# Performance work log

Hardware: AMD Instinct MI355X
Metric: run time of the kernel (lower is better)

The kernel has to match this reference:

```python
import jax, jax.numpy as jnp
import numpy as np

RADIUS = 0.3
NEIGHBOR_LIMIT = 32
LN_EPS = 1e-5


def setup_inputs() -> dict:
    key = jax.random.key(0)
    k0, k1, k2 = jax.random.split(key, 3)
    N, C = 16384, 256
    pts = jax.random.normal(k0, (N, 3), jnp.float32)
    masks = jnp.ones((N,), dtype=bool)  # all queries active (fixed shape for jit)
    feats = jax.random.normal(k1, (N, C), jnp.float32)
    W = jax.random.normal(k2, (C, C), jnp.float32) * (1.0 / np.sqrt(C))
    b = jnp.zeros((C,), jnp.float32)
    gamma = jnp.ones((C,), jnp.float32)
    beta = jnp.zeros((C,), jnp.float32)
    return {
        "shifted_src_points_c": pts,
        "src_masks": masks,
        "src_feats_c": feats,
        "W": W,
        "b": b,
        "gamma": gamma,
        "beta": beta,
    }


def _ball_query(q, s, radius, k):
    # squared pairwise distances via the ||q||^2 + ||s||^2 - 2 q.s^T identity
    # (avoids the [N, N, 3] broadcast intermediate)
    q2 = jnp.sum(q * q, axis=-1, keepdims=True)        # [Q, 1]
    s2 = jnp.sum(s * s, axis=-1)                        # [N]
    d2 = q2 + s2[None, :] - 2.0 * (q @ s.T)             # [Q, N]
    neg_d2, idx = jax.lax.top_k(-d2, k)                 # k nearest neighbors
    # out-of-radius slots get index 0, matching the original
    # `neighbor_indices[neighbor_indices == N] = 0` padding replacement
    idx = jnp.where(-neg_d2 > radius * radius, 0, idx)
    return idx                                          # [Q, k] int32


def reference(shifted_src_points_c, src_masks, src_feats_c, W, b, gamma, beta):
    # src_masks is all-True by construction -> queries == all points
    q_nodes = shifted_src_points_c
    idx = _ball_query(q_nodes, shifted_src_points_c, RADIUS, NEIGHBOR_LIMIT)
    group = src_feats_c[idx]                            # [Q, K, C] irregular gather
    pooled = jnp.max(group, axis=1)                     # max over neighbors -> [Q, C]
    h = pooled @ W.T + b                                # nn.Linear(256, 256)
    mu = jnp.mean(h, axis=-1, keepdims=True)
    var = jnp.var(h, axis=-1, keepdims=True)
    h = (h - mu) * jax.lax.rsqrt(var + LN_EPS) * gamma + beta  # LayerNorm
    return jax.nn.relu(h)
```

## Files before the change

kernel.cpp:

```cpp
#include <hip/hip_runtime.h>
#include <stdint.h>

#define NPTS 16384
#define CFEAT 256
#define KNN 32
#define RR_HI 0.0900101f
#define NC 21
#define NCELLS (NC * NC * NC)
#define NPAD 9264
#define INVW 3.3332222f
#define NBUCK 128

typedef __attribute__((ext_vector_type(8))) short short8;
typedef __attribute__((ext_vector_type(4))) float floatx4;

__device__ __forceinline__ uint32_t f2bf(uint32_t u) {
  return (u + 0x7fffu + ((u >> 16) & 1u)) >> 16;
}
__device__ __forceinline__ int cell1d(float x) {
  int c = (int)floorf((x + 3.15f) * INVW);
  return min(max(c, 0), NC - 1);
}

__global__ __launch_bounds__(256) void k_prep(const float* __restrict__ feats,
                                              uint16_t* __restrict__ featsb,
                                              const float* __restrict__ Wm,
                                              uint16_t* __restrict__ Wb,
                                              const float* __restrict__ pts,
                                              uint32_t* __restrict__ cellcnt) {
  const int b = blockIdx.x, t = threadIdx.x;
  if (b < 4096) {
    const int i = b * 256 + t;
    const uint4 u = ((const uint4*)feats)[i];
    const uint32_t lo = f2bf(u.x) | (f2bf(u.y) << 16);
    const uint32_t hi = f2bf(u.z) | (f2bf(u.w) << 16);
    ((uint2*)featsb)[i] = make_uint2(lo, hi);
  } else {
    const int i = (b - 4096) * 256 + t;
    const uint4 u = ((const uint4*)Wm)[i];
    const uint32_t lo = f2bf(u.x) | (f2bf(u.y) << 16);
    const uint32_t hi = f2bf(u.z) | (f2bf(u.w) << 16);
    ((uint2*)Wb)[i] = make_uint2(lo, hi);
    const int cx = cell1d(pts[3 * i]), cy = cell1d(pts[3 * i + 1]), cz = cell1d(pts[3 * i + 2]);
    atomicAdd(&cellcnt[(cz * NC + cy) * NC + cx], 1u);
  }
}

__global__ __launch_bounds__(1024) void k_scan(const uint32_t* __restrict__ hist,
                                               uint32_t* __restrict__ start, int n) {
  __shared__ uint32_t wsum[16];
  __shared__ uint32_t carry;
  const int t = threadIdx.x, wv = t >> 6, ln = t & 63;
  if (t == 0) carry = 0;
  __syncthreads();
  const int nq = n >> 2;
  for (int qb = 0; qb < nq; qb += 4096) {
    uint4 v[4];
    uint32_t psum[4];
    uint32_t tot = 0;
    #pragma unroll
    for (int k = 0; k < 4; ++k) {
      const int i4 = qb + t * 4 + k;
      v[k] = (i4 < nq) ? ((const uint4*)hist)[i4] : make_uint4(0, 0, 0, 0);
      psum[k] = tot;
      tot += v[k].x + v[k].y + v[k].z + v[k].w;
    }
    uint32_t s = tot;
    #pragma unroll
    for (int off = 1; off < 64; off <<= 1) {
      uint32_t o = __shfl_up(s, off, 64);
      if (ln >= off) s += o;
    }
    if (ln == 63) wsum[wv] = s;
    const uint32_t cbase = carry;
    __syncthreads();
    uint32_t woff = 0;
    for (int w = 0; w < wv; ++w) woff += wsum[w];
    const uint32_t base = cbase + woff + s - tot;
    #pragma unroll
    for (int k = 0; k < 4; ++k) {
      const int i4 = qb + t * 4 + k;
      if (i4 < nq) {
        const uint32_t e = base + psum[k];
        ((uint4*)start)[i4] =
            make_uint4(e, e + v[k].x, e + v[k].x + v[k].y, e + v[k].x + v[k].y + v[k].z);
      }
    }
    __syncthreads();
    if (t == 1023) carry = base + tot;
    __syncthreads();
  }
  if (t == 0) start[n] = carry;
}

__global__ __launch_bounds__(256) void k_scatter(const float* __restrict__ pts,
                                                 const uint32_t* __restrict__ cellstart,
                                                 uint32_t* __restrict__ cellptr,
                                                 uint32_t* __restrict__ sortedq,
                                                 float4* __restrict__ sortedpts) {
  const int i = blockIdx.x * 256 + threadIdx.x;
  const float x = pts[3 * i], y = pts[3 * i + 1], z = pts[3 * i + 2];
  const int c = (cell1d(z) * NC + cell1d(y)) * NC + cell1d(x);
  const uint32_t pos = cellstart[c] + atomicAdd(&cellptr[c], 1u);
  sortedq[pos] = (uint32_t)i;
  sortedpts[pos] = make_float4(x, y, z, __uint_as_float((uint32_t)i));
}

__global__ __launch_bounds__(256) void k_fsp(const uint32_t* __restrict__ sortedq,
                                             const uint32_t* __restrict__ cellstart,
                                             const float4* __restrict__ sortedpts,
                                             const uint16_t* __restrict__ featsb,
                                             uint16_t* __restrict__ pooledb) {
  __shared__ uint64_t keys[4][256];
  __shared__ uint32_t hist[4][NBUCK];
  __shared__ uint32_t sids[4][KNN];
  const int t = threadIdx.x;
  const int w = t >> 6;
  const int lane = t & 63;
  const uint64_t ltmask = (1ull << lane) - 1ull;
  const int q = (int)sortedq[blockIdx.x * 4 + w];
  const float4 qp = sortedpts[blockIdx.x * 4 + w];
  const float qx = qp.x, qy = qp.y, qz = qp.z;
  const int icx = cell1d(qx), icy = cell1d(qy), icz = cell1d(qz);
  const int x0 = max(icx - 1, 0), x1 = min(icx + 1, NC - 1);
  int S[9], E[9];
  #pragma unroll
  for (int r = 0; r < 9; ++r) {
    const int cz = icz + (r / 3) - 1;
    const int cy = icy + (r % 3) - 1;
    const bool ok = (cz >= 0) && (cz < NC) && (cy >= 0) && (cy < NC);
    const int rb = ((ok ? cz : 0) * NC + (ok ? cy : 0)) * NC;
    const int s = (int)cellstart[rb + x0];
    const int e = (int)cellstart[rb + x1 + 1];
    S[r] = ok ? s : 0;
    E[r] = ok ? e : 0;
  }
  int PRE[10], OFF[9];
  PRE[0] = 0;
  #pragma unroll
  for (int r = 0; r < 9; ++r) {
    PRE[r + 1] = PRE[r] + (E[r] - S[r]);
    OFF[r] = S[r] - PRE[r];
  }
  const int total = PRE[9];
  uint32_t c_run = 0;
  for (int v0 = 0; v0 < total; v0 += 64) {
    const int v = v0 + lane;
    int addr = v + OFF[0];
    #pragma unroll
    for (int r = 1; r < 9; ++r) addr = (v >= PRE[r]) ? (v + OFF[r]) : addr;
    const int ia = min(addr, NPTS - 1);
    const float4 p = sortedpts[ia];
    const float dxf = qx - p.x, dyf = qy - p.y, dzf = qz - p.z;
    const float d2 = __fmaf_rn(dxf, dxf, __fmaf_rn(dyf, dyf, __fmul_rn(dzf, dzf)));
    bool pass = (v < total) && (d2 <= RR_HI);
    uint64_t key = 0;
    if (pass) {
      const double ddx = (double)qx - (double)p.x;
      const double ddy = (double)qy - (double)p.y;
      const double ddz = (double)qz - (double)p.z;
      const double dd2 = fma(ddx, ddx, fma(ddy, ddy, ddz * ddz));
      pass = (dd2 <= 0.3 * 0.3);
      key = ((uint64_t)__double_as_longlong(dd2) & ~0x3FFFull) |
            (uint64_t)__float_as_uint(p.w);
    }
    const uint64_t mask = __ballot(pass);
    if (pass) {
      const uint32_t pos = c_run + (uint32_t)__popcll(mask & ltmask);
      if (pos < 256u) keys[w][pos] = key;
    }
    c_run += (uint32_t)__popcll(mask);
  }
  const int c = (int)min(c_run, 256u);
  if (c <= KNN) {
    if (lane < KNN) sids[w][lane] = (lane < c) ? (uint32_t)(keys[w][lane] & 0x3FFFull) : 0u;
  } else {
    const uint64_t INVALID = ~0ull;
    uint64_t k0 = (lane < c) ? keys[w][lane] : INVALID;
    uint64_t k1 = (lane + 64 < c) ? keys[w][lane + 64] : INVALID;
    uint64_t k2 = (lane + 128 < c) ? keys[w][lane + 128] : INVALID;
    uint64_t k3 = (lane + 192 < c) ? keys[w][lane + 192] : INVALID;
    hist[w][lane] = 0;
    hist[w][lane + 64] = 0;
    int b0 = 999, b1 = 999, b2 = 999, b3 = 999;
    const float bs = 128.0f / 0.09f;
    if (k0 != INVALID) { b0 = min(NBUCK - 1, (int)((float)__longlong_as_double((long long)(k0 & ~0x3FFFull)) * bs)); atomicAdd(&hist[w][b0], 1u); }
    if (k1 != INVALID) { b1 = min(NBUCK - 1, (int)((float)__longlong_as_double((long long)(k1 & ~0x3FFFull)) * bs)); atomicAdd(&hist[w][b1], 1u); }
    if (k2 != INVALID) { b2 = min(NBUCK - 1, (int)((float)__longlong_as_double((long long)(k2 & ~0x3FFFull)) * bs)); atomicAdd(&hist[w][b2], 1u); }
    if (k3 != INVALID) { b3 = min(NBUCK - 1, (int)((float)__longlong_as_double((long long)(k3 & ~0x3FFFull)) * bs)); atomicAdd(&hist[w][b3], 1u); }
    const uint32_t h0 = hist[w][2 * lane], h1 = hist[w][2 * lane + 1];
    const uint32_t tot = h0 + h1;
    uint32_t s = tot;
    #pragma unroll
    for (int off = 1; off < 64; off <<= 1) {
      uint32_t o = __shfl_up(s, off, 64);
      if (lane >= off) s += o;
    }
    const uint32_t C0 = s - tot + h0;
    const uint32_t C1 = s - tot + h0 + h1;
    const uint64_t me = __ballot(C0 >= KNN);
    const uint64_t mo = __ballot(C1 >= KNN);
    const int be = me ? 2 * (__ffsll((unsigned long long)me) - 1) : (1 << 30);
    const int bo = mo ? 2 * (__ffsll((unsigned long long)mo) - 1) + 1 : (1 << 30);
    const int bstar = min(be, bo);
    const uint32_t mval_mine = (bstar & 1) ? (C1 - h1) : (C0 - h0);
    const uint32_t m = (uint32_t)__shfl((int)mval_mine, bstar >> 1, 64);
    uint32_t wpos = 0;
    {
      bool win = (b0 < bstar);
      uint64_t bm = __ballot(win);
      if (win) sids[w][wpos + (uint32_t)__popcll(bm & ltmask)] = (uint32_t)(k0 & 0x3FFFull);
      wpos += (uint32_t)__popcll(bm);
      win = (b1 < bstar); bm = __ballot(win);
      if (win) sids[w][wpos + (uint32_t)__popcll(bm & ltmask)] = (uint32_t)(k1 & 0x3FFFull);
      wpos += (uint32_t)__popcll(bm);
      win = (b2 < bstar); bm = __ballot(win);
      if (win) sids[w][wpos + (uint32_t)__popcll(bm & ltmask)] = (uint32_t)(k2 & 0x3FFFull);
      wpos += (uint32_t)__popcll(bm);
      win = (b3 < bstar); bm = __ballot(win);
      if (win) sids[w][wpos + (uint32_t)__popcll(bm & ltmask)] = (uint32_t)(k3 & 0x3FFFull);
      wpos += (uint32_t)__popcll(bm);
    }
    uint64_t e0 = (b0 == bstar) ? k0 : INVALID;
    uint64_t e1 = (b1 == bstar) ? k1 : INVALID;
    uint64_t e2 = (b2 == bstar) ? k2 : INVALID;
    uint64_t e3 = (b3 == bstar) ? k3 : INVALID;
    const int need = KNN - (int)m;
    for (int it = 0; it < need; ++it) {
      uint64_t a = e0 < e1 ? e0 : e1;
      uint64_t b = e2 < e3 ? e2 : e3;
      uint64_t mn = a < b ? a : b;
      #pragma unroll
      for (int off = 1; off < 64; off <<= 1) {
        uint64_t o = (uint64_t)__shfl_xor((unsigned long long)mn, off, 64);
        mn = o < mn ? o : mn;
      }
      if (e0 == mn) e0 = INVALID;
      else if (e1 == mn) e1 = INVALID;
      else if (e2 == mn) e2 = INVALID;
      else if (e3 == mn) e3 = INVALID;
      if (lane == 0) sids[w][m + it] = (uint32_t)(mn & 0x3FFFull);
    }
  }
  float m0 = -3.0e38f, m1 = -3.0e38f, m2 = -3.0e38f, m3 = -3.0e38f;
  float m4 = -3.0e38f, m5 = -3.0e38f, m6 = -3.0e38f, m7 = -3.0e38f;
  const int half = lane >> 5, l31 = lane & 31;
  #pragma unroll 4
  for (int k = 0; k < KNN / 2; ++k) {
    const uint32_t idx = sids[w][2 * k + half];
    const uint4 v = *(const uint4*)(featsb + (size_t)idx * CFEAT + l31 * 8);
    m0 = fmaxf(m0, __uint_as_float(v.x << 16));
    m1 = fmaxf(m1, __uint_as_float(v.x & 0xffff0000u));
    m2 = fmaxf(m2, __uint_as_float(v.y << 16));
    m3 = fmaxf(m3, __uint_as_float(v.y & 0xffff0000u));
    m4 = fmaxf(m4, __uint_as_float(v.z << 16));
    m5 = fmaxf(m5, __uint_as_float(v.z & 0xffff0000u));
    m6 = fmaxf(m6, __uint_as_float(v.w << 16));
    m7 = fmaxf(m7, __uint_as_float(v.w & 0xffff0000u));
  }
  m0 = fmaxf(m0, __shfl_xor(m0, 32, 64));
  m1 = fmaxf(m1, __shfl_xor(m1, 32, 64));
  m2 = fmaxf(m2, __shfl_xor(m2, 32, 64));
  m3 = fmaxf(m3, __shfl_xor(m3, 32, 64));
  m4 = fmaxf(m4, __shfl_xor(m4, 32, 64));
  m5 = fmaxf(m5, __shfl_xor(m5, 32, 64));
  m6 = fmaxf(m6, __shfl_xor(m6, 32, 64));
  m7 = fmaxf(m7, __shfl_xor(m7, 32, 64));
  if (half == 0) {
    uint4 o;
    o.x = (__float_as_uint(m0) >> 16) | (__float_as_uint(m1) & 0xffff0000u);
    o.y = (__float_as_uint(m2) >> 16) | (__float_as_uint(m3) & 0xffff0000u);
    o.z = (__float_as_uint(m4) >> 16) | (__float_as_uint(m5) & 0xffff0000u);
    o.w = (__float_as_uint(m6) >> 16) | (__float_as_uint(m7) & 0xffff0000u);
    ((uint4*)(pooledb + (size_t)q * CFEAT))[l31] = o;
  }
}

__global__ __launch_bounds__(256) void k_gemm_ln(const uint16_t* __restrict__ pooledb,
                                                 const uint16_t* __restrict__ Wb,
                                                 const float* __restrict__ bias,
                                                 const float* __restrict__ gamma,
                                                 const float* __restrict__ beta,
                                                 float* __restrict__ out) {
  __shared__ uint16_t As[64 * 264];
  __shared__ uint16_t Bs[256 * 40];
  __shared__ float red1[4][64];
  __shared__ float red2[4][64];
  __shared__ float mu_s[64];
  __shared__ float rs_s[64];
  const int t = threadIdx.x;
  const int wave = t >> 6;
  const int lane = t & 63;
  const int quad = lane >> 4;
  const int l15 = lane & 15;
  const int m0 = blockIdx.x * 64;
  {
    const int m = t >> 2, qtr = t & 3;
    const uint4* src = (const uint4*)(pooledb + (size_t)(m0 + m) * 256 + qtr * 64);
    uint4* dst = (uint4*)(As + m * 264 + qtr * 64);
    #pragma unroll
    for (int i = 0; i < 8; ++i) dst[i] = src[i];
  }
  floatx4 acc[4][4];
  #pragma unroll
  for (int mi = 0; mi < 4; ++mi)
    #pragma unroll
    for (int ni = 0; ni < 4; ++ni)
      acc[mi][ni] = (floatx4){0.f, 0.f, 0.f, 0.f};

  for (int step = 0; step < 8; ++step) {
    __syncthreads();
    {
      const uint4* src = (const uint4*)(Wb + (size_t)t * 256 + step * 32);
      uint4* dst = (uint4*)(Bs + t * 40);
      #pragma unroll
      for (int i = 0; i < 4; ++i) dst[i] = src[i];
    }
    __syncthreads();
    short8 a[4], b[4];
    #pragma unroll
    for (int mi = 0; mi < 4; ++mi)
      a[mi] = *(const short8*)(As + (mi * 16 + l15) * 264 + step * 32 + quad * 8);
    #pragma unroll
    for (int ni = 0; ni < 4; ++ni)
      b[ni] = *(const short8*)(Bs + (wave * 64 + ni * 16 + l15) * 40 + quad * 8);
    #pragma unroll
    for (int mi = 0; mi < 4; ++mi)
      #pragma unroll
      for (int ni = 0; ni < 4; ++ni)
        acc[mi][ni] = __builtin_amdgcn_mfma_f32_16x16x32_bf16(a[mi], b[ni], acc[mi][ni], 0, 0, 0);
  }

  float bcol[4], gcol[4], zcol[4];
  #pragma unroll
  for (int ni = 0; ni < 4; ++ni) {
    const int col = wave * 64 + ni * 16 + l15;
    bcol[ni] = bias[col];
    gcol[ni] = gamma[col];
    zcol[ni] = beta[col];
  }
  #pragma unroll
  for (int mi = 0; mi < 4; ++mi)
    #pragma unroll
    for (int ni = 0; ni < 4; ++ni)
      #pragma unroll
      for (int r = 0; r < 4; ++r)
        acc[mi][ni][r] += bcol[ni];
  #pragma unroll
  for (int mi = 0; mi < 4; ++mi) {
    #pragma unroll
    for (int r = 0; r < 4; ++r) {
      const float v0 = acc[mi][0][r], v1 = acc[mi][1][r], v2 = acc[mi][2][r], v3 = acc[mi][3][r];
      float s1 = v0 + v1 + v2 + v3;
      float s2 = v0 * v0 + v1 * v1 + v2 * v2 + v3 * v3;
      #pragma unroll
      for (int off = 1; off < 16; off <<= 1) {
        s1 += __shfl_xor(s1, off, 64);
        s2 += __shfl_xor(s2, off, 64);
      }
      if (l15 == 0) {
        const int row = mi * 16 + quad * 4 + r;
        red1[wave][row] = s1;
        red2[wave][row] = s2;
      }
    }
  }
  __syncthreads();
  if (t < 64) {
    const float s1 = red1[0][t] + red1[1][t] + red1[2][t] + red1[3][t];
    const float s2 = red2[0][t] + red2[1][t] + red2[2][t] + red2[3][t];
    const float mu = s1 * (1.0f / 256.0f);
    const float var = s2 * (1.0f / 256.0f) - mu * mu;
    mu_s[t] = mu;
    rs_s[t] = 1.0f / sqrtf(var + 1e-5f);
  }
  __syncthreads();
  #pragma unroll
  for (int mi = 0; mi < 4; ++mi) {
    #pragma unroll
    for (int r = 0; r < 4; ++r) {
      const int row = mi * 16 + quad * 4 + r;
      const float mu = mu_s[row], rs = rs_s[row];
      #pragma unroll
      for (int ni = 0; ni < 4; ++ni) {
        float y = (acc[mi][ni][r] - mu) * rs * gcol[ni] + zcol[ni];
        out[(size_t)(m0 + row) * 256 + wave * 64 + ni * 16 + l15] = fmaxf(y, 0.0f);
      }
    }
  }
}

extern "C" void kernel_launch(void* const* d_in, const int* in_sizes, int n_in,
                              void* d_out, int out_size, void* d_ws, size_t ws_size,
                              hipStream_t stream) {
  (void)in_sizes; (void)n_in; (void)out_size; (void)ws_size;
  const float* pts   = (const float*)d_in[0];
  const float* feats = (const float*)d_in[2];
  const float* Wm    = (const float*)d_in[3];
  const float* bias  = (const float*)d_in[4];
  const float* gamma = (const float*)d_in[5];
  const float* beta  = (const float*)d_in[6];
  float* out = (float*)d_out;

  uint8_t* ws = (uint8_t*)d_ws;
  uint16_t* featsb    = (uint16_t*)ws;
  uint16_t* Wb        = (uint16_t*)(ws + 8388608);
  uint16_t* pooledb   = (uint16_t*)(ws + 8519680);
  uint32_t* cellcnt   = (uint32_t*)(ws + 16908288);
  uint32_t* cellptr   = (uint32_t*)(ws + 16945408);
  uint32_t* cellstart = (uint32_t*)(ws + 16982528);
  uint32_t* sortedq   = (uint32_t*)(ws + 17019648);
  float4*   sortedpts = (float4*)(ws + 17085184);

  (void)hipMemsetAsync(cellcnt, 0, 2 * 37120, stream);
  k_prep<<<4160, 256, 0, stream>>>(feats, featsb, Wm, Wb, pts, cellcnt);
  k_scan<<<1, 1024, 0, stream>>>(cellcnt, cellstart, NPAD);
  k_scatter<<<64, 256, 0, stream>>>(pts, cellstart, cellptr, sortedq, sortedpts);
  k_fsp<<<4096, 256, 0, stream>>>(sortedq, cellstart, sortedpts, featsb, pooledb);
  k_gemm_ln<<<256, 256, 0, stream>>>(pooledb, Wb, bias, gamma, beta, out);
}
```

Measured before the change: 135.8 us.

## Fuse histogram, scan and scatter into one single-block LDS counting-sort kernel

The global atomic histogram, memset, scan kernel and scatter kernel are replaced by one 1024-thread kernel. It builds the cell histogram in shared memory from per-point cell ids written by the prep kernel, scans it, and scatters points using shared-memory atomics. This removes two launches and a memset, along with the global atomics. In exchange, the scatter step runs on a single workgroup. The query coordinates converted to double are also hoisted out of the neighbor loop.

```diff
diff --git a/kernel.cpp b/kernel.cpp
--- a/kernel.cpp
+++ b/kernel.cpp
@@ -27,7 +27,7 @@
                                               const float* __restrict__ Wm,
                                               uint16_t* __restrict__ Wb,
                                               const float* __restrict__ pts,
-                                              uint32_t* __restrict__ cellcnt) {
+                                              uint32_t* __restrict__ cellid) {
   const int b = blockIdx.x, t = threadIdx.x;
   if (b < 4096) {
     const int i = b * 256 + t;
@@ -42,68 +42,66 @@
     const uint32_t hi = f2bf(u.z) | (f2bf(u.w) << 16);
     ((uint2*)Wb)[i] = make_uint2(lo, hi);
     const int cx = cell1d(pts[3 * i]), cy = cell1d(pts[3 * i + 1]), cz = cell1d(pts[3 * i + 2]);
-    atomicAdd(&cellcnt[(cz * NC + cy) * NC + cx], 1u);
-  }
-}
-
-__global__ __launch_bounds__(1024) void k_scan(const uint32_t* __restrict__ hist,
-                                               uint32_t* __restrict__ start, int n) {
+    cellid[i] = (uint32_t)((cz * NC + cy) * NC + cx);
+  }
+}
+
+__global__ __launch_bounds__(1024) void k_hss(const float* __restrict__ pts,
+                                              const uint32_t* __restrict__ cellid,
+                                              uint32_t* __restrict__ cellstart,
+                                              uint32_t* __restrict__ sortedq,
+                                              float4* __restrict__ sortedpts) {
+  __shared__ uint32_t cnt[NPAD];
   __shared__ uint32_t wsum[16];
-  __shared__ uint32_t carry;
   const int t = threadIdx.x, wv = t >> 6, ln = t & 63;
-  if (t == 0) carry = 0;
-  __syncthreads();
-  const int nq = n >> 2;
-  for (int qb = 0; qb < nq; qb += 4096) {
-    uint4 v[4];
-    uint32_t psum[4];
-    uint32_t tot = 0;
-    #pragma unroll
-    for (int k = 0; k < 4; ++k) {
-      const int i4 = qb + t * 4 + k;
-      v[k] = (i4 < nq) ? ((const uint4*)hist)[i4] : make_uint4(0, 0, 0, 0);
-      psum[k] = tot;
-      tot += v[k].x + v[k].y + v[k].z + v[k].w;
-    }
-    uint32_t s = tot;
-    #pragma unroll
-    for (int off = 1; off < 64; off <<= 1) {
-      uint32_t o = __shfl_up(s, off, 64);
-      if (ln >= off) s += o;
-    }
-    if (ln == 63) wsum[wv] = s;
-    const uint32_t cbase = carry;
-    __syncthreads();
-    uint32_t woff = 0;
-    for (int w = 0; w < wv; ++w) woff += wsum[w];
-    const uint32_t base = cbase + woff + s - tot;
-    #pragma unroll
-    for (int k = 0; k < 4; ++k) {
-      const int i4 = qb + t * 4 + k;
-      if (i4 < nq) {
-        const uint32_t e = base + psum[k];
-        ((uint4*)start)[i4] =
-            make_uint4(e, e + v[k].x, e + v[k].x + v[k].y, e + v[k].x + v[k].y + v[k].z);
-      }
-    }
-    __syncthreads();
-    if (t == 1023) carry = base + tot;
-    __syncthreads();
-  }
-  if (t == 0) start[n] = carry;
-}
-
-__global__ __launch_bounds__(256) void k_scatter(const float* __restrict__ pts,
-                                                 const uint32_t* __restrict__ cellstart,
-                                                 uint32_t* __restrict__ cellptr,
-                                                 uint32_t* __restrict__ sortedq,
-                                                 float4* __restrict__ sortedpts) {
-  const int i = blockIdx.x * 256 + threadIdx.x;
-  const float x = pts[3 * i], y = pts[3 * i + 1], z = pts[3 * i + 2];
-  const int c = (cell1d(z) * NC + cell1d(y)) * NC + cell1d(x);
-  const uint32_t pos = cellstart[c] + atomicAdd(&cellptr[c], 1u);
-  sortedq[pos] = (uint32_t)i;
-  sortedpts[pos] = make_float4(x, y, z, __uint_as_float((uint32_t)i));
+  for (int i = t; i < NPAD; i += 1024) cnt[i] = 0;
+  __syncthreads();
+  uint32_t cid[16];
+  #pragma unroll
+  for (int k = 0; k < 16; ++k) {
+    const int p = k * 1024 + t;
+    cid[k] = cellid[p];
+    atomicAdd(&cnt[cid[k]], 1u);
+  }
+  __syncthreads();
+  uint32_t loc[10];
+  uint32_t tsum = 0;
+  #pragma unroll
+  for (int k = 0; k < 10; ++k) {
+    const int idx = t * 10 + k;
+    loc[k] = (idx < NPAD) ? cnt[idx] : 0;
+    tsum += loc[k];
+  }
+  uint32_t s = tsum;
+  #pragma unroll
+  for (int off = 1; off < 64; off <<= 1) {
+    uint32_t o = __shfl_up(s, off, 64);
+    if (ln >= off) s += o;
+  }
+  if (ln == 63) wsum[wv] = s;
+  __syncthreads();
+  uint32_t woff = 0;
+  for (int w = 0; w < wv; ++w) woff += wsum[w];
+  uint32_t run = woff + s - tsum;
+  #pragma unroll
+  for (int k = 0; k < 10; ++k) {
+    const int idx = t * 10 + k;
+    if (idx < NPAD) {
+      cellstart[idx] = run;
+      cnt[idx] = run;
+      run += loc[k];
+    }
+  }
+  if (t == 0) cellstart[NPAD] = NPTS;
+  __syncthreads();
+  #pragma unroll
+  for (int k = 0; k < 16; ++k) {
+    const int p = k * 1024 + t;
+    const uint32_t pos = atomicAdd(&cnt[cid[k]], 1u);
+    const float x = pts[3 * p], y = pts[3 * p + 1], z = pts[3 * p + 2];
+    sortedq[pos] = (uint32_t)p;
+    sortedpts[pos] = make_float4(x, y, z, __uint_as_float((uint32_t)p));
+  }
 }
 
 __global__ __launch_bounds__(256) void k_fsp(const uint32_t* __restrict__ sortedq,
@@ -121,6 +119,7 @@
   const int q = (int)sortedq[blockIdx.x * 4 + w];
   const float4 qp = sortedpts[blockIdx.x * 4 + w];
   const float qx = qp.x, qy = qp.y, qz = qp.z;
+  const double dqx = (double)qx, dqy = (double)qy, dqz = (double)qz;
   const int icx = cell1d(qx), icy = cell1d(qy), icz = cell1d(qz);
   const int x0 = max(icx - 1, 0), x1 = min(icx + 1, NC - 1);
   int S[9], E[9];
@@ -156,9 +155,9 @@
     bool pass = (v < total) && (d2 <= RR_HI);
     uint64_t key = 0;
     if (pass) {
-      const double ddx = (double)qx - (double)p.x;
-      const double ddy = (double)qy - (double)p.y;
-      const double ddz = (double)qz - (double)p.z;
+      const double ddx = dqx - (double)p.x;
+      const double ddy = dqy - (double)p.y;
+      const double ddz = dqz - (double)p.z;
       const double dd2 = fma(ddx, ddx, fma(ddy, ddy, ddz * ddz));
       pass = (dd2 <= 0.3 * 0.3);
       key = ((uint64_t)__double_as_longlong(dd2) & ~0x3FFFull) |
@@ -406,16 +405,13 @@
   uint16_t* featsb    = (uint16_t*)ws;
   uint16_t* Wb        = (uint16_t*)(ws + 8388608);
   uint16_t* pooledb   = (uint16_t*)(ws + 8519680);
-  uint32_t* cellcnt   = (uint32_t*)(ws + 16908288);
-  uint32_t* cellptr   = (uint32_t*)(ws + 16945408);
-  uint32_t* cellstart = (uint32_t*)(ws + 16982528);
-  uint32_t* sortedq   = (uint32_t*)(ws + 17019648);
-  float4*   sortedpts = (float4*)(ws + 17085184);
-
-  (void)hipMemsetAsync(cellcnt, 0, 2 * 37120, stream);
-  k_prep<<<4160, 256, 0, stream>>>(feats, featsb, Wm, Wb, pts, cellcnt);
-  k_scan<<<1, 1024, 0, stream>>>(cellcnt, cellstart, NPAD);
-  k_scatter<<<64, 256, 0, stream>>>(pts, cellstart, cellptr, sortedq, sortedpts);
+  uint32_t* cellid    = (uint32_t*)(ws + 16908288);
+  uint32_t* cellstart = (uint32_t*)(ws + 16973824);
+  uint32_t* sortedq   = (uint32_t*)(ws + 17010944);
+  float4*   sortedpts = (float4*)(ws + 17076480);
+
+  k_prep<<<4160, 256, 0, stream>>>(feats, featsb, Wm, Wb, pts, cellid);
+  k_hss<<<1, 1024, 0, stream>>>(pts, cellid, cellstart, sortedq, sortedpts);
   k_fsp<<<4096, 256, 0, stream>>>(sortedq, cellstart, sortedpts, featsb, pooledb);
   k_gemm_ln<<<256, 256, 0, stream>>>(pooledb, Wb, bias, gamma, beta, out);
 }
```

Result: slower. 159.2 us (+17.2%).
